# Kernel optimization log

Hardware: AMD Instinct MI355X
Metric: run time of the kernel (lower is better)

Reference implementation:

```python
import jax, jax.numpy as jnp
import numpy as np

N, E, F_IN, H, L = 1536, 49152, 27, 64, 32


def _ln(x, g, b, eps=1e-5):
    m = x.mean(-1, keepdims=True)
    v = ((x - m) ** 2).mean(-1, keepdims=True)
    return (x - m) * jax.lax.rsqrt(v + eps) * g + b


def _gatv2(x, src, dst, Wl, bl, Wr, br, att, bias, n):
    # PyG GATv2Conv, heads=1: alpha_ij = softmax_j( att . leaky_relu(Wl x_j + Wr x_i) )
    xl = x @ Wl + bl  # source transform [n,H]
    xr = x @ Wr + br  # target transform [n,H]
    e = jax.nn.leaky_relu(xl[src] + xr[dst], 0.2)  # [E',H]
    s = e @ att  # [E'] attention logits
    m = jax.ops.segment_max(s, dst, num_segments=n)
    w = jnp.exp(s - m[dst])
    denom = jax.ops.segment_sum(w, dst, num_segments=n)
    alpha = w / denom[dst]
    return jax.ops.segment_sum(alpha[:, None] * xl[src], dst, num_segments=n) + bias


def _model(x, eps_nodes, eps_graph, edge_index,
           Wl1, bl1, Wr1, br1, att1, bias1,
           Wl2, bl2, Wr2, br2, att2, bias2,
           Wnm, bnm, Wnv, bnv, Wgm, bgm, Wgv, bgv,
           Wd1, bd1, ln1_g, ln1_b, Wd2, bd2, ln2_g, ln2_b, Wd3, bd3,
           We1, be1, lne_g, lne_b, We2, be2,
           Wf1, bf1, lnf_g, lnf_b, Wf2, bf2):
    n = x.shape[0]
    loop = jnp.arange(n)
    src = jnp.concatenate([edge_index[0], loop])  # add self loops (PyG default)
    dst = jnp.concatenate([edge_index[1], loop])
    h = jax.nn.relu(_gatv2(x, src, dst, Wl1, bl1, Wr1, br1, att1, bias1, n))
    h = jax.nn.relu(_gatv2(h, src, dst, Wl2, bl2, Wr2, br2, att2, bias2, n))
    node_mu = h @ Wnm + bnm
    node_logvar = h @ Wnv + bnv
    gh = h.mean(0)
    graph_mu = gh @ Wgm + bgm
    graph_logvar = gh @ Wgv + bgv
    z = node_mu + eps_nodes * jnp.exp(0.5 * node_logvar)  # node reparam (training)
    _zg = graph_mu + eps_graph * jnp.exp(0.5 * graph_logvar)  # z_graph: computed, unused downstream as in source
    # dec_node_features MLP
    nf = _ln(jax.nn.relu(z @ Wd1 + bd1), ln1_g, ln1_b)
    nf = _ln(jax.nn.relu(nf @ Wd2 + bd2), ln2_g, ln2_b)
    nf = nf @ Wd3 + bd3  # [n, F_IN]
    # feature_refinement (node_embeddings = h is passed in forward)
    nf = _ln(jax.nn.relu(jnp.concatenate([nf, h], -1) @ Wf1 + bf1), lnf_g, lnf_b)
    node_features = nf @ Wf2 + bf2
    # edge_pred over all i<j pairs, vectorized (replaces the O(N^2) python loop)
    iu, ju = jnp.triu_indices(n, k=1)
    ei = jnp.concatenate([z[iu], z[ju]], -1)  # [P, 2L]
    eh = _ln(jax.nn.relu(ei @ We1 + be1), lne_g, lne_b)
    edge_logits = (eh @ We2 + be2)[:, 0]  # [P]
    return node_features, edge_logits, node_mu, node_logvar, graph_mu, graph_logvar


def setup_inputs() -> dict:
    key = jax.random.key(0)
    ki = iter(jax.random.split(key, 40))
    def W(fi, fo):
        return jax.random.normal(next(ki), (fi, fo), jnp.float32) / np.sqrt(fi)
    z64 = jnp.zeros((H,), jnp.float32)
    o64 = jnp.ones((H,), jnp.float32)
    zL = jnp.zeros((L,), jnp.float32)
    zF = jnp.zeros((F_IN,), jnp.float32)
    inp = {}
    inp["x"] = jax.random.normal(next(ki), (N, F_IN), jnp.float32)
    inp["edge_index"] = jax.random.randint(next(ki), (2, E), 0, N)
    inp["eps_nodes"] = jax.random.normal(next(ki), (N, L), jnp.float32)
    inp["eps_graph"] = jax.random.normal(next(ki), (L,), jnp.float32)
    inp.update(Wl1=W(F_IN, H), bl1=z64, Wr1=W(F_IN, H), br1=z64,
               att1=jax.random.normal(next(ki), (H,), jnp.float32) / np.sqrt(H), bias1=z64,
               Wl2=W(H, H), bl2=z64, Wr2=W(H, H), br2=z64,
               att2=jax.random.normal(next(ki), (H,), jnp.float32) / np.sqrt(H), bias2=z64)
    inp.update(Wnm=W(H, L), bnm=zL, Wnv=W(H, L), bnv=zL,
               Wgm=W(H, L), bgm=zL, Wgv=W(H, L), bgv=zL)
    inp.update(Wd1=W(L, H), bd1=z64, ln1_g=o64, ln1_b=z64,
               Wd2=W(H, H), bd2=z64, ln2_g=o64, ln2_b=z64,
               Wd3=W(H, F_IN), bd3=zF)
    inp.update(We1=W(2 * L, H), be1=z64, lne_g=o64, lne_b=z64,
               We2=W(H, 1), be2=jnp.zeros((1,), jnp.float32))
    inp.update(Wf1=W(F_IN + H, H), bf1=z64, lnf_g=o64, lnf_b=z64,
               Wf2=W(H, F_IN), bf2=zF)
    return inp


def reference(x, edge_index, eps_nodes, eps_graph,
              Wl1, bl1, Wr1, br1, att1, bias1,
              Wl2, bl2, Wr2, br2, att2, bias2,
              Wnm, bnm, Wnv, bnv, Wgm, bgm, Wgv, bgv,
              Wd1, bd1, ln1_g, ln1_b, Wd2, bd2, ln2_g, ln2_b, Wd3, bd3,
              We1, be1, lne_g, lne_b, We2, be2,
              Wf1, bf1, lnf_g, lnf_b, Wf2, bf2):
    return _model(x, eps_nodes, eps_graph, edge_index,
                  Wl1, bl1, Wr1, br1, att1, bias1,
                  Wl2, bl2, Wr2, br2, att2, bias2,
                  Wnm, bnm, Wnv, bnv, Wgm, bgm, Wgv, bgv,
                  Wd1, bd1, ln1_g, ln1_b, Wd2, bd2, ln2_g, ln2_b, Wd3, bd3,
                  We1, be1, lne_g, lne_b, We2, be2,
                  Wf1, bf1, lnf_g, lnf_b, Wf2, bf2)
```

## Files before the change

kernel.cpp:

```cpp
#include <hip/hip_runtime.h>

#define NN 1536
#define NE 49152
#define NM (NE + NN)
#define FIN 27
#define HD 64
#define LDIM 32
#define PP 1178880

#define EL_OFF  (NN*FIN)
#define MU_OFF  (EL_OFF + PP)
#define LV_OFF  (MU_OFF + NN*LDIM)
#define GMU_OFF (LV_OFF + NN*LDIM)
#define GLV_OFF (GMU_OFF + LDIM)

__device__ __forceinline__ float wsum(float v) {
#pragma unroll
  for (int m = 1; m < 64; m <<= 1) v += __shfl_xor(v, m, 64);
  return v;
}
__device__ __forceinline__ void wsum2(float& a, float& b) {
#pragma unroll
  for (int m = 1; m < 64; m <<= 1) {
    a += __shfl_xor(a, m, 64);
    b += __shfl_xor(b, m, 64);
  }
}
__device__ __forceinline__ float lnorm64(float x, float g, float b) {
  float s1 = x, s2 = x * x;
  wsum2(s1, s2);
  float mu = s1 * (1.0f / 64.0f);
  float var = fmaf(-mu, mu, s2 * (1.0f / 64.0f));
  return (x - mu) * rsqrtf(var + 1e-5f) * g + b;
}
__device__ __forceinline__ void cp4(float* dst, const float* __restrict__ src,
                                    int n4, int t) {
  const float4* s4 = (const float4*)src;
  float4* d4 = (float4*)dst;
  for (int e = t; e < n4; e += 256) d4[e] = s4[e];
}

template <int KIN, bool FUSE>
__global__ __launch_bounds__(256) void gvae_xform(
    const float* __restrict__ in, const float* __restrict__ Dn,
    const float* __restrict__ hbias,
    const float* __restrict__ Wl, const float* __restrict__ bl,
    const float* __restrict__ Wr, const float* __restrict__ br,
    float* __restrict__ xl, float* __restrict__ xr) {
  __shared__ __align__(16) float sWl[KIN * HD];
  __shared__ __align__(16) float sWr[KIN * HD];
  int t = threadIdx.x;
  cp4(sWl, Wl, KIN * 16, t);
  cp4(sWr, Wr, KIN * 16, t);
  int i = blockIdx.x * 4 + (t >> 6);
  int k = t & 63;
  float xv = (k < KIN) ? in[i * KIN + k] : 0.f;
  if (FUSE) xv = fmaxf(xv / Dn[i] + hbias[k], 0.f);
  float l0 = bl[k], l1 = 0.f, r0 = br[k], r1 = 0.f;
  __syncthreads();
#pragma unroll
  for (int a = 0; a < KIN; a += 2) {
    float xa = __shfl(xv, a, 64);
    l0 = fmaf(xa, sWl[a * HD + k], l0);
    r0 = fmaf(xa, sWr[a * HD + k], r0);
    if (a + 1 < KIN) {
      float xb = __shfl(xv, a + 1, 64);
      l1 = fmaf(xb, sWl[(a + 1) * HD + k], l1);
      r1 = fmaf(xb, sWr[(a + 1) * HD + k], r1);
    }
  }
  xl[i * HD + k] = l0 + l1;
  xr[i * HD + k] = r0 + r1;
}

__global__ __launch_bounds__(256) void gvae_edgepass(
    const int* __restrict__ ei,
    const float* __restrict__ xl, const float* __restrict__ xr,
    const float* __restrict__ att,
    float* __restrict__ A, float* __restrict__ D) {
  int m = blockIdx.x * 4 + (threadIdx.x >> 6);
  int lane = threadIdx.x & 63;
  int src, dst;
  if (m < NE) { src = ei[m]; dst = ei[NE + m]; }
  else        { src = m - NE; dst = m - NE; }
  float xls = xl[src * HD + lane];
  float e = xls + xr[dst * HD + lane];
  e = fmaxf(e, 0.2f * e);
  float w = expf(wsum(e * att[lane]));
  atomicAdd(&A[dst * HD + lane], w * xls);
  if (lane == 0) atomicAdd(&D[dst], w);
}

#define oNM 0
#define oNV 2048
#define oE1 4096
#define oD1 8192
#define oD2 10240
#define oD3 14336
#define oF1 16064
#define oF2 21888
#define SWTOT 23616

__global__ __launch_bounds__(256) void gvae_node(
    const float* __restrict__ A2, const float* __restrict__ D2,
    const float* __restrict__ bias2,
    const float* __restrict__ eps,
    const float* __restrict__ Wnm, const float* __restrict__ bnm,
    const float* __restrict__ Wnv, const float* __restrict__ bnv,
    const float* __restrict__ We1, const float* __restrict__ be1,
    const float* __restrict__ Wd1, const float* __restrict__ bd1,
    const float* __restrict__ g1, const float* __restrict__ b1,
    const float* __restrict__ Wd2, const float* __restrict__ bd2,
    const float* __restrict__ g2, const float* __restrict__ b2,
    const float* __restrict__ Wd3, const float* __restrict__ bd3,
    const float* __restrict__ Wf1, const float* __restrict__ bf1,
    const float* __restrict__ gf, const float* __restrict__ bfv,
    const float* __restrict__ Wf2, const float* __restrict__ bf2,
    float* __restrict__ uo, float* __restrict__ vo,
    float* __restrict__ gh, float* __restrict__ out) {
  __shared__ __align__(16) float sW[SWTOT];
  __shared__ float ghred[256];
  int t = threadIdx.x;
  cp4(sW + oNM, Wnm, 512, t);
  cp4(sW + oNV, Wnv, 512, t);
  cp4(sW + oE1, We1, 1024, t);
  cp4(sW + oD1, Wd1, 512, t);
  cp4(sW + oD2, Wd2, 1024, t);
  cp4(sW + oD3, Wd3, 432, t);
  cp4(sW + oF1, Wf1, 1456, t);
  cp4(sW + oF2, Wf2, 432, t);

  int i = blockIdx.x * 4 + (t >> 6);
  int k = t & 63;
  int kk = k & 31;
  int kc = (k < FIN) ? k : (FIN - 1);
  float h2k = fmaxf(A2[i * HD + k] / D2[i] + bias2[k], 0.f);
  ghred[t] = h2k;
  __syncthreads();
  if (t < 64) {
    float s = (ghred[t] + ghred[t + 64]) + (ghred[t + 128] + ghred[t + 192]);
    atomicAdd(&gh[t], s * (1.0f / NN));
  }

  const float* W = sW + ((k < 32) ? oNM : oNV);
  float c0 = (k < 32) ? bnm[kk] : bnv[kk];
  float c1 = 0.f, c2 = 0.f, c3 = 0.f;
#pragma unroll
  for (int a = 0; a < HD; a += 4) {
    c0 = fmaf(__shfl(h2k, a, 64),     W[a * LDIM + kk],       c0);
    c1 = fmaf(__shfl(h2k, a + 1, 64), W[(a + 1) * LDIM + kk], c1);
    c2 = fmaf(__shfl(h2k, a + 2, 64), W[(a + 2) * LDIM + kk], c2);
    c3 = fmaf(__shfl(h2k, a + 3, 64), W[(a + 3) * LDIM + kk], c3);
  }
  float acc = (c0 + c1) + (c2 + c3);
  if (k < 32) out[MU_OFF + i * LDIM + kk] = acc;
  else        out[LV_OFF + i * LDIM + kk] = acc;

  float lv = __shfl(acc, k + 32, 64);
  float zk = acc + eps[i * LDIM + kk] * expf(0.5f * lv);

  float u0 = be1[k], u1 = 0.f, v0 = 0.f, v1 = 0.f;
#pragma unroll
  for (int a = 0; a < LDIM; a += 2) {
    float za = __shfl(zk, a, 64);
    float zb = __shfl(zk, a + 1, 64);
    u0 = fmaf(za, sW[oE1 + a * HD + k], u0);
    u1 = fmaf(zb, sW[oE1 + (a + 1) * HD + k], u1);
    v0 = fmaf(za, sW[oE1 + (a + LDIM) * HD + k], v0);
    v1 = fmaf(zb, sW[oE1 + (a + 1 + LDIM) * HD + k], v1);
  }
  uo[i * HD + k] = u0 + u1;
  vo[i * HD + k] = v0 + v1;

  c0 = bd1[k]; c1 = 0.f; c2 = 0.f; c3 = 0.f;
#pragma unroll
  for (int a = 0; a < LDIM; a += 4) {
    c0 = fmaf(__shfl(zk, a, 64),     sW[oD1 + a * HD + k],       c0);
    c1 = fmaf(__shfl(zk, a + 1, 64), sW[oD1 + (a + 1) * HD + k], c1);
    c2 = fmaf(__shfl(zk, a + 2, 64), sW[oD1 + (a + 2) * HD + k], c2);
    c3 = fmaf(__shfl(zk, a + 3, 64), sW[oD1 + (a + 3) * HD + k], c3);
  }
  float nf1 = lnorm64(fmaxf((c0 + c1) + (c2 + c3), 0.f), g1[k], b1[k]);

  c0 = bd2[k]; c1 = 0.f; c2 = 0.f; c3 = 0.f;
#pragma unroll
  for (int a = 0; a < HD; a += 4) {
    c0 = fmaf(__shfl(nf1, a, 64),     sW[oD2 + a * HD + k],       c0);
    c1 = fmaf(__shfl(nf1, a + 1, 64), sW[oD2 + (a + 1) * HD + k], c1);
    c2 = fmaf(__shfl(nf1, a + 2, 64), sW[oD2 + (a + 2) * HD + k], c2);
    c3 = fmaf(__shfl(nf1, a + 3, 64), sW[oD2 + (a + 3) * HD + k], c3);
  }
  float nf2 = lnorm64(fmaxf((c0 + c1) + (c2 + c3), 0.f), g2[k], b2[k]);

  c0 = 0.f; c1 = 0.f; c2 = 0.f; c3 = 0.f;
#pragma unroll
  for (int a = 0; a < HD; a += 4) {
    c0 = fmaf(__shfl(nf2, a, 64),     sW[oD3 + a * FIN + kc],       c0);
    c1 = fmaf(__shfl(nf2, a + 1, 64), sW[oD3 + (a + 1) * FIN + kc], c1);
    c2 = fmaf(__shfl(nf2, a + 2, 64), sW[oD3 + (a + 2) * FIN + kc], c2);
    c3 = fmaf(__shfl(nf2, a + 3, 64), sW[oD3 + (a + 3) * FIN + kc], c3);
  }
  float nf3 = (k < FIN) ? ((c0 + c1) + (c2 + c3) + bd3[kc]) : 0.f;

  c0 = bf1[k]; c1 = 0.f; c2 = 0.f; c3 = 0.f;
#pragma unroll
  for (int j = 0; j < FIN; j++) {
    float nj = __shfl(nf3, j, 64);
    c0 = fmaf(nj, sW[oF1 + j * HD + k], c0);
  }
#pragma unroll
  for (int a = 0; a < HD; a += 4) {
    c0 = fmaf(__shfl(h2k, a, 64),     sW[oF1 + (FIN + a) * HD + k],     c0);
    c1 = fmaf(__shfl(h2k, a + 1, 64), sW[oF1 + (FIN + a + 1) * HD + k], c1);
    c2 = fmaf(__shfl(h2k, a + 2, 64), sW[oF1 + (FIN + a + 2) * HD + k], c2);
    c3 = fmaf(__shfl(h2k, a + 3, 64), sW[oF1 + (FIN + a + 3) * HD + k], c3);
  }
  float rr = lnorm64(fmaxf((c0 + c1) + (c2 + c3), 0.f), gf[k], bfv[k]);

  c0 = 0.f; c1 = 0.f; c2 = 0.f; c3 = 0.f;
#pragma unroll
  for (int a = 0; a < HD; a += 4) {
    c0 = fmaf(__shfl(rr, a, 64),     sW[oF2 + a * FIN + kc],       c0);
    c1 = fmaf(__shfl(rr, a + 1, 64), sW[oF2 + (a + 1) * FIN + kc], c1);
    c2 = fmaf(__shfl(rr, a + 2, 64), sW[oF2 + (a + 2) * FIN + kc], c2);
    c3 = fmaf(__shfl(rr, a + 3, 64), sW[oF2 + (a + 3) * FIN + kc], c3);
  }
  if (k < FIN) out[i * FIN + k] = (c0 + c1) + (c2 + c3) + bf2[kc];
}

__global__ void gvae_ghead(const float* __restrict__ gh,
                           const float* __restrict__ Wgm, const float* __restrict__ bgm,
                           const float* __restrict__ Wgv, const float* __restrict__ bgv,
                           float* __restrict__ out) {
  int k = threadIdx.x;
  int kk = k & 31;
  float ghk = gh[k];
  const float* W = (k < 32) ? Wgm : Wgv;
  float c0 = (k < 32) ? bgm[kk] : bgv[kk];
  float c1 = 0.f, c2 = 0.f, c3 = 0.f;
#pragma unroll
  for (int a = 0; a < HD; a += 4) {
    c0 = fmaf(__shfl(ghk, a, 64),     W[a * LDIM + kk],       c0);
    c1 = fmaf(__shfl(ghk, a + 1, 64), W[(a + 1) * LDIM + kk], c1);
    c2 = fmaf(__shfl(ghk, a + 2, 64), W[(a + 2) * LDIM + kk], c2);
    c3 = fmaf(__shfl(ghk, a + 3, 64), W[(a + 3) * LDIM + kk], c3);
  }
  float acc = (c0 + c1) + (c2 + c3);
  if (k < 32) out[GMU_OFF + kk] = acc;
  else        out[GLV_OFF + kk] = acc;
}

__global__ __launch_bounds__(256) void gvae_edge(
    const float* __restrict__ u, const float* __restrict__ v,
    const float* __restrict__ lng, const float* __restrict__ lnb,
    const float* __restrict__ w2, const float* __restrict__ be2,
    float* __restrict__ out) {
  int bj = blockIdx.x, bi = blockIdx.y;
  if (bi > bj) return;
  __shared__ float U[64 * 64];
  __shared__ float V[64 * 68];
  __shared__ float C[64];
  __shared__ float cc[2];
  int t = threadIdx.x;
  const float4* u4p = (const float4*)(u + bi * 64 * HD);
  const float4* v4p = (const float4*)(v + bj * 64 * HD);
#pragma unroll
  for (int it = 0; it < 4; ++it) {
    int r = t + it * 256;
    int row = r >> 4, q = r & 15;
    float4 uu = u4p[r];
    *(float4*)&U[row * 64 + q * 4] = uu;
    float4 vv = v4p[r];
    *(float4*)&V[row * 68 + q * 4] = vv;
  }
  if (t < 64) {
    float ck = lng[t] * w2[t];
    C[t] = ck;
    float cb = lnb[t] * w2[t];
    float sC = wsum(ck);
    float sB = wsum(cb);
    if (t == 0) { cc[0] = sC; cc[1] = sB + be2[0]; }
  }
  __syncthreads();
  float C1 = cc[0], C0 = cc[1];

  int w = t >> 6, lane = t & 63;
  float S1[16], S2[16], Sc[16];
#pragma unroll
  for (int ii = 0; ii < 16; ii++) { S1[ii] = 0.f; S2[ii] = 0.f; Sc[ii] = 0.f; }
  const float* Ub = &U[(w * 16) * 64];
  for (int k4 = 0; k4 < 16; k4++) {
    float4 v4 = *(const float4*)&V[lane * 68 + k4 * 4];
    float4 c4 = *(const float4*)&C[k4 * 4];
#pragma unroll
    for (int ii = 0; ii < 16; ii++) {
      float4 u4 = *(const float4*)&Ub[ii * 64 + k4 * 4];
      float t0 = fmaxf(u4.x + v4.x, 0.f);
      float t1 = fmaxf(u4.y + v4.y, 0.f);
      float t2 = fmaxf(u4.z + v4.z, 0.f);
      float t3 = fmaxf(u4.w + v4.w, 0.f);
      S1[ii] += (t0 + t1) + (t2 + t3);
      S2[ii] = fmaf(t0, t0, fmaf(t1, t1, fmaf(t2, t2, fmaf(t3, t3, S2[ii]))));
      Sc[ii] = fmaf(t0, c4.x, fmaf(t1, c4.y, fmaf(t2, c4.z, fmaf(t3, c4.w, Sc[ii]))));
    }
  }
  int j = bj * 64 + lane;
  const float inv64 = 1.0f / 64.0f;
#pragma unroll
  for (int ii = 0; ii < 16; ii++) {
    int i = bi * 64 + w * 16 + ii;
    if (j > i) {
      int pbase = i * (2 * NN - i - 1) / 2 - i - 1;
      float mu = S1[ii] * inv64;
      float var = fmaf(-mu, mu, S2[ii] * inv64);
      float logit = (Sc[ii] - mu * C1) * rsqrtf(var + 1e-5f) + C0;
      out[pbase + j] = logit;
    }
  }
}

extern "C" void kernel_launch(void* const* d_in, const int* in_sizes, int n_in,
                              void* d_out, int out_size, void* d_ws, size_t ws_size,
                              hipStream_t stream) {
  const float* x    = (const float*)d_in[0];
  const int*   ei   = (const int*)d_in[1];
  const float* eps  = (const float*)d_in[2];
  const float* Wl1  = (const float*)d_in[4];
  const float* bl1  = (const float*)d_in[5];
  const float* Wr1  = (const float*)d_in[6];
  const float* br1  = (const float*)d_in[7];
  const float* att1 = (const float*)d_in[8];
  const float* bias1= (const float*)d_in[9];
  const float* Wl2  = (const float*)d_in[10];
  const float* bl2  = (const float*)d_in[11];
  const float* Wr2  = (const float*)d_in[12];
  const float* br2  = (const float*)d_in[13];
  const float* att2 = (const float*)d_in[14];
  const float* bias2= (const float*)d_in[15];
  const float* Wnm  = (const float*)d_in[16];
  const float* bnm  = (const float*)d_in[17];
  const float* Wnv  = (const float*)d_in[18];
  const float* bnv  = (const float*)d_in[19];
  const float* Wgm  = (const float*)d_in[20];
  const float* bgm  = (const float*)d_in[21];
  const float* Wgv  = (const float*)d_in[22];
  const float* bgv  = (const float*)d_in[23];
  const float* Wd1  = (const float*)d_in[24];
  const float* bd1  = (const float*)d_in[25];
  const float* ln1g = (const float*)d_in[26];
  const float* ln1b = (const float*)d_in[27];
  const float* Wd2  = (const float*)d_in[28];
  const float* bd2  = (const float*)d_in[29];
  const float* ln2g = (const float*)d_in[30];
  const float* ln2b = (const float*)d_in[31];
  const float* Wd3  = (const float*)d_in[32];
  const float* bd3  = (const float*)d_in[33];
  const float* We1  = (const float*)d_in[34];
  const float* be1  = (const float*)d_in[35];
  const float* lneg = (const float*)d_in[36];
  const float* lneb = (const float*)d_in[37];
  const float* We2  = (const float*)d_in[38];
  const float* be2  = (const float*)d_in[39];
  const float* Wf1  = (const float*)d_in[40];
  const float* bf1  = (const float*)d_in[41];
  const float* lnfg = (const float*)d_in[42];
  const float* lnfb = (const float*)d_in[43];
  const float* Wf2  = (const float*)d_in[44];
  const float* bf2  = (const float*)d_in[45];
  float* out = (float*)d_out;

  float* fb  = (float*)d_ws;
  float* xl1 = fb;
  float* xr1 = xl1 + NN * HD;
  float* xl2 = xr1 + NN * HD;
  float* xr2 = xl2 + NN * HD;
  float* uu  = xr2 + NN * HD;
  float* vv  = uu  + NN * HD;
  float* A1  = vv  + NN * HD;
  float* A2  = A1  + NN * HD;
  float* D1  = A2  + NN * HD;
  float* D2  = D1  + NN;
  float* gh  = D2  + NN;
  size_t zbytes = (size_t)(2 * NN * HD + 2 * NN + HD) * sizeof(float);

  hipMemsetAsync(A1, 0, zbytes, stream);

  gvae_xform<FIN, false><<<NN / 4, 256, 0, stream>>>(x, nullptr, nullptr,
                                                     Wl1, bl1, Wr1, br1, xl1, xr1);
  gvae_edgepass<<<NM / 4, 256, 0, stream>>>(ei, xl1, xr1, att1, A1, D1);
  gvae_xform<HD, true><<<NN / 4, 256, 0, stream>>>(A1, D1, bias1,
                                                   Wl2, bl2, Wr2, br2, xl2, xr2);
  gvae_edgepass<<<NM / 4, 256, 0, stream>>>(ei, xl2, xr2, att2, A2, D2);

  gvae_node<<<NN / 4, 256, 0, stream>>>(A2, D2, bias2, eps,
      Wnm, bnm, Wnv, bnv, We1, be1,
      Wd1, bd1, ln1g, ln1b, Wd2, bd2, ln2g, ln2b, Wd3, bd3,
      Wf1, bf1, lnfg, lnfb, Wf2, bf2,
      uu, vv, gh, out);
  gvae_ghead<<<1, 64, 0, stream>>>(gh, Wgm, bgm, Wgv, bgv, out);
  gvae_edge<<<dim3(24, 24), 256, 0, stream>>>(uu, vv, lneg, lneb, We2, be2, out + EL_OFF);
}
```

Measured before the change: 259.7 us.

## Fuse all stages into one persistent cooperative kernel with grid syncs

Measured after the change: 990.6 us. 3.81x slower.

```diff
diff --git a/kernel.cpp b/kernel.cpp
--- a/kernel.cpp
+++ b/kernel.cpp
@@ -1,4 +1,7 @@
 #include <hip/hip_runtime.h>
+#include <hip/hip_cooperative_groups.h>
+
+namespace cg = cooperative_groups;
 
 #define NN 1536
 #define NE 49152
@@ -33,370 +36,345 @@
   float var = fmaf(-mu, mu, s2 * (1.0f / 64.0f));
   return (x - mu) * rsqrtf(var + 1e-5f) * g + b;
 }
-__device__ __forceinline__ void cp4(float* dst, const float* __restrict__ src,
-                                    int n4, int t) {
-  const float4* s4 = (const float4*)src;
-  float4* d4 = (float4*)dst;
-  for (int e = t; e < n4; e += 256) d4[e] = s4[e];
-}
-
-template <int KIN, bool FUSE>
-__global__ __launch_bounds__(256) void gvae_xform(
-    const float* __restrict__ in, const float* __restrict__ Dn,
-    const float* __restrict__ hbias,
-    const float* __restrict__ Wl, const float* __restrict__ bl,
-    const float* __restrict__ Wr, const float* __restrict__ br,
-    float* __restrict__ xl, float* __restrict__ xr) {
-  __shared__ __align__(16) float sWl[KIN * HD];
-  __shared__ __align__(16) float sWr[KIN * HD];
-  int t = threadIdx.x;
-  cp4(sWl, Wl, KIN * 16, t);
-  cp4(sWr, Wr, KIN * 16, t);
-  int i = blockIdx.x * 4 + (t >> 6);
-  int k = t & 63;
-  float xv = (k < KIN) ? in[i * KIN + k] : 0.f;
-  if (FUSE) xv = fmaxf(xv / Dn[i] + hbias[k], 0.f);
-  float l0 = bl[k], l1 = 0.f, r0 = br[k], r1 = 0.f;
-  __syncthreads();
-#pragma unroll
-  for (int a = 0; a < KIN; a += 2) {
-    float xa = __shfl(xv, a, 64);
-    l0 = fmaf(xa, sWl[a * HD + k], l0);
-    r0 = fmaf(xa, sWr[a * HD + k], r0);
-    if (a + 1 < KIN) {
-      float xb = __shfl(xv, a + 1, 64);
-      l1 = fmaf(xb, sWl[(a + 1) * HD + k], l1);
-      r1 = fmaf(xb, sWr[(a + 1) * HD + k], r1);
-    }
-  }
-  xl[i * HD + k] = l0 + l1;
-  xr[i * HD + k] = r0 + r1;
-}
-
-__global__ __launch_bounds__(256) void gvae_edgepass(
-    const int* __restrict__ ei,
-    const float* __restrict__ xl, const float* __restrict__ xr,
-    const float* __restrict__ att,
-    float* __restrict__ A, float* __restrict__ D) {
-  int m = blockIdx.x * 4 + (threadIdx.x >> 6);
-  int lane = threadIdx.x & 63;
-  int src, dst;
-  if (m < NE) { src = ei[m]; dst = ei[NE + m]; }
-  else        { src = m - NE; dst = m - NE; }
-  float xls = xl[src * HD + lane];
-  float e = xls + xr[dst * HD + lane];
-  e = fmaxf(e, 0.2f * e);
-  float w = expf(wsum(e * att[lane]));
-  atomicAdd(&A[dst * HD + lane], w * xls);
-  if (lane == 0) atomicAdd(&D[dst], w);
-}
-
-#define oNM 0
-#define oNV 2048
-#define oE1 4096
-#define oD1 8192
-#define oD2 10240
-#define oD3 14336
-#define oF1 16064
-#define oF2 21888
-#define SWTOT 23616
-
-__global__ __launch_bounds__(256) void gvae_node(
-    const float* __restrict__ A2, const float* __restrict__ D2,
-    const float* __restrict__ bias2,
-    const float* __restrict__ eps,
-    const float* __restrict__ Wnm, const float* __restrict__ bnm,
-    const float* __restrict__ Wnv, const float* __restrict__ bnv,
-    const float* __restrict__ We1, const float* __restrict__ be1,
-    const float* __restrict__ Wd1, const float* __restrict__ bd1,
-    const float* __restrict__ g1, const float* __restrict__ b1,
-    const float* __restrict__ Wd2, const float* __restrict__ bd2,
-    const float* __restrict__ g2, const float* __restrict__ b2,
-    const float* __restrict__ Wd3, const float* __restrict__ bd3,
-    const float* __restrict__ Wf1, const float* __restrict__ bf1,
-    const float* __restrict__ gf, const float* __restrict__ bfv,
-    const float* __restrict__ Wf2, const float* __restrict__ bf2,
-    float* __restrict__ uo, float* __restrict__ vo,
-    float* __restrict__ gh, float* __restrict__ out) {
-  __shared__ __align__(16) float sW[SWTOT];
-  __shared__ float ghred[256];
-  int t = threadIdx.x;
-  cp4(sW + oNM, Wnm, 512, t);
-  cp4(sW + oNV, Wnv, 512, t);
-  cp4(sW + oE1, We1, 1024, t);
-  cp4(sW + oD1, Wd1, 512, t);
-  cp4(sW + oD2, Wd2, 1024, t);
-  cp4(sW + oD3, Wd3, 432, t);
-  cp4(sW + oF1, Wf1, 1456, t);
-  cp4(sW + oF2, Wf2, 432, t);
-
-  int i = blockIdx.x * 4 + (t >> 6);
-  int k = t & 63;
-  int kk = k & 31;
-  int kc = (k < FIN) ? k : (FIN - 1);
-  float h2k = fmaxf(A2[i * HD + k] / D2[i] + bias2[k], 0.f);
-  ghred[t] = h2k;
-  __syncthreads();
+
+struct GP {
+  const float* x; const int* ei; const float* eps;
+  const float *Wl1, *bl1, *Wr1, *br1, *att1, *bias1;
+  const float *Wl2, *bl2, *Wr2, *br2, *att2, *bias2;
+  const float *Wnm, *bnm, *Wnv, *bnv, *Wgm, *bgm, *Wgv, *bgv;
+  const float *Wd1, *bd1, *g1, *b1, *Wd2, *bd2, *g2, *b2, *Wd3, *bd3;
+  const float *We1, *be1, *lng, *lnb, *w2, *be2;
+  const float *Wf1, *bf1, *gf, *bfv, *Wf2, *bf2;
+  float *xl1, *xr1, *xl2, *xr2, *uu, *vv;
+  float *A1, *A2, *D1, *D2, *gh;
+  float* out;
+};
+
+__global__ __launch_bounds__(256, 4) void gvae_mono(GP p) {
+  cg::grid_group grid = cg::this_grid();
+  __shared__ __align__(16) float sh[8516];
+  const int t = threadIdx.x, b = blockIdx.x;
+  const int NB = gridDim.x;
+  const int wv = t >> 6, lane = t & 63;
+  const int WSTRIDE = NB * 4;
+
+  {
+    float4* z4 = (float4*)p.A1;
+    const int nz4 = (2 * NN * HD + 2 * NN + HD) / 4;
+    float4 zz = {0.f, 0.f, 0.f, 0.f};
+    for (int e = b * 256 + t; e < nz4; e += NB * 256) z4[e] = zz;
+    float bl = p.bl1[lane], br = p.br1[lane];
+    for (int i = b + NB * wv; i < NN; i += WSTRIDE) {
+      float xv = (lane < FIN) ? p.x[i * FIN + lane] : 0.f;
+      float l0 = bl, l1 = 0.f, r0 = br, r1 = 0.f;
+#pragma unroll
+      for (int a = 0; a < FIN; a += 2) {
+        float xa = __shfl(xv, a, 64);
+        l0 = fmaf(xa, p.Wl1[a * HD + lane], l0);
+        r0 = fmaf(xa, p.Wr1[a * HD + lane], r0);
+        if (a + 1 < FIN) {
+          float xb = __shfl(xv, a + 1, 64);
+          l1 = fmaf(xb, p.Wl1[(a + 1) * HD + lane], l1);
+          r1 = fmaf(xb, p.Wr1[(a + 1) * HD + lane], r1);
+        }
+      }
+      p.xl1[i * HD + lane] = l0 + l1;
+      p.xr1[i * HD + lane] = r0 + r1;
+    }
+  }
+  __threadfence();
+  grid.sync();
+
+  {
+    float ak = p.att1[lane];
+    for (int m = b + NB * wv; m < NM; m += WSTRIDE) {
+      int src, dst;
+      if (m < NE) { src = p.ei[m]; dst = p.ei[NE + m]; }
+      else        { src = m - NE; dst = src; }
+      float xls = p.xl1[src * HD + lane];
+      float e = xls + p.xr1[dst * HD + lane];
+      e = fmaxf(e, 0.2f * e);
+      float w = expf(wsum(e * ak));
+      atomicAdd(&p.A1[dst * HD + lane], w * xls);
+      if (lane == 0) atomicAdd(&p.D1[dst], w);
+    }
+  }
+  __threadfence();
+  grid.sync();
+
+  {
+    float hb = p.bias1[lane], bl = p.bl2[lane], br = p.br2[lane];
+    for (int i = b + NB * wv; i < NN; i += WSTRIDE) {
+      float xv = fmaxf(p.A1[i * HD + lane] / p.D1[i] + hb, 0.f);
+      float l0 = bl, l1 = 0.f, r0 = br, r1 = 0.f;
+#pragma unroll
+      for (int a = 0; a < HD; a += 2) {
+        float xa = __shfl(xv, a, 64);
+        float xb = __shfl(xv, a + 1, 64);
+        l0 = fmaf(xa, p.Wl2[a * HD + lane], l0);
+        r0 = fmaf(xa, p.Wr2[a * HD + lane], r0);
+        l1 = fmaf(xb, p.Wl2[(a + 1) * HD + lane], l1);
+        r1 = fmaf(xb, p.Wr2[(a + 1) * HD + lane], r1);
+      }
+      p.xl2[i * HD + lane] = l0 + l1;
+      p.xr2[i * HD + lane] = r0 + r1;
+    }
+  }
+  __threadfence();
+  grid.sync();
+
+  {
+    float ak = p.att2[lane];
+    for (int m = b + NB * wv; m < NM; m += WSTRIDE) {
+      int src, dst;
+      if (m < NE) { src = p.ei[m]; dst = p.ei[NE + m]; }
+      else        { src = m - NE; dst = src; }
+      float xls = p.xl2[src * HD + lane];
+      float e = xls + p.xr2[dst * HD + lane];
+      e = fmaxf(e, 0.2f * e);
+      float w = expf(wsum(e * ak));
+      atomicAdd(&p.A2[dst * HD + lane], w * xls);
+      if (lane == 0) atomicAdd(&p.D2[dst], w);
+    }
+  }
+  __threadfence();
+  grid.sync();
+
+  {
+    const int k = lane, kk = k & 31;
+    const int kc = (k < FIN) ? k : (FIN - 1);
+    for (int i = b + NB * wv; i < NN; i += WSTRIDE) {
+      float h2k = fmaxf(p.A2[i * HD + k] / p.D2[i] + p.bias2[k], 0.f);
+      atomicAdd(&p.gh[k], h2k * (1.0f / NN));
+
+      const float* W = (k < 32) ? p.Wnm : p.Wnv;
+      float c0 = (k < 32) ? p.bnm[kk] : p.bnv[kk];
+      float c1 = 0.f, c2 = 0.f, c3 = 0.f;
+#pragma unroll
+      for (int a = 0; a < HD; a += 4) {
+        c0 = fmaf(__shfl(h2k, a, 64),     W[a * LDIM + kk],       c0);
+        c1 = fmaf(__shfl(h2k, a + 1, 64), W[(a + 1) * LDIM + kk], c1);
+        c2 = fmaf(__shfl(h2k, a + 2, 64), W[(a + 2) * LDIM + kk], c2);
+        c3 = fmaf(__shfl(h2k, a + 3, 64), W[(a + 3) * LDIM + kk], c3);
+      }
+      float acc = (c0 + c1) + (c2 + c3);
+      if (k < 32) p.out[MU_OFF + i * LDIM + kk] = acc;
+      else        p.out[LV_OFF + i * LDIM + kk] = acc;
+
+      float lv = __shfl(acc, k + 32, 64);
+      float zk = acc + p.eps[i * LDIM + kk] * expf(0.5f * lv);
+
+      float u0 = p.be1[k], u1 = 0.f, v0 = 0.f, v1 = 0.f;
+#pragma unroll
+      for (int a = 0; a < LDIM; a += 2) {
+        float za = __shfl(zk, a, 64);
+        float zb = __shfl(zk, a + 1, 64);
+        u0 = fmaf(za, p.We1[a * HD + k], u0);
+        u1 = fmaf(zb, p.We1[(a + 1) * HD + k], u1);
+        v0 = fmaf(za, p.We1[(a + LDIM) * HD + k], v0);
+        v1 = fmaf(zb, p.We1[(a + 1 + LDIM) * HD + k], v1);
+      }
+      p.uu[i * HD + k] = u0 + u1;
+      p.vv[i * HD + k] = v0 + v1;
+
+      c0 = p.bd1[k]; c1 = 0.f; c2 = 0.f; c3 = 0.f;
+#pragma unroll
+      for (int a = 0; a < LDIM; a += 4) {
+        c0 = fmaf(__shfl(zk, a, 64),     p.Wd1[a * HD + k],       c0);
+        c1 = fmaf(__shfl(zk, a + 1, 64), p.Wd1[(a + 1) * HD + k], c1);
+        c2 = fmaf(__shfl(zk, a + 2, 64), p.Wd1[(a + 2) * HD + k], c2);
+        c3 = fmaf(__shfl(zk, a + 3, 64), p.Wd1[(a + 3) * HD + k], c3);
+      }
+      float nf1 = lnorm64(fmaxf((c0 + c1) + (c2 + c3), 0.f), p.g1[k], p.b1[k]);
+
+      c0 = p.bd2[k]; c1 = 0.f; c2 = 0.f; c3 = 0.f;
+#pragma unroll
+      for (int a = 0; a < HD; a += 4) {
+        c0 = fmaf(__shfl(nf1, a, 64),     p.Wd2[a * HD + k],       c0);
+        c1 = fmaf(__shfl(nf1, a + 1, 64), p.Wd2[(a + 1) * HD + k], c1);
+        c2 = fmaf(__shfl(nf1, a + 2, 64), p.Wd2[(a + 2) * HD + k], c2);
+        c3 = fmaf(__shfl(nf1, a + 3, 64), p.Wd2[(a + 3) * HD + k], c3);
+      }
+      float nf2 = lnorm64(fmaxf((c0 + c1) + (c2 + c3), 0.f), p.g2[k], p.b2[k]);
+
+      c0 = 0.f; c1 = 0.f; c2 = 0.f; c3 = 0.f;
+#pragma unroll
+      for (int a = 0; a < HD; a += 4) {
+        c0 = fmaf(__shfl(nf2, a, 64),     p.Wd3[a * FIN + kc],       c0);
+        c1 = fmaf(__shfl(nf2, a + 1, 64), p.Wd3[(a + 1) * FIN + kc], c1);
+        c2 = fmaf(__shfl(nf2, a + 2, 64), p.Wd3[(a + 2) * FIN + kc], c2);
+        c3 = fmaf(__shfl(nf2, a + 3, 64), p.Wd3[(a + 3) * FIN + kc], c3);
+      }
+      float nf3 = (k < FIN) ? ((c0 + c1) + (c2 + c3) + p.bd3[kc]) : 0.f;
+
+      c0 = p.bf1[k]; c1 = 0.f; c2 = 0.f; c3 = 0.f;
+#pragma unroll
+      for (int j = 0; j < FIN; j++) {
+        float nj = __shfl(nf3, j, 64);
+        c0 = fmaf(nj, p.Wf1[j * HD + k], c0);
+      }
+#pragma unroll
+      for (int a = 0; a < HD; a += 4) {
+        c0 = fmaf(__shfl(h2k, a, 64),     p.Wf1[(FIN + a) * HD + k],     c0);
+        c1 = fmaf(__shfl(h2k, a + 1, 64), p.Wf1[(FIN + a + 1) * HD + k], c1);
+        c2 = fmaf(__shfl(h2k, a + 2, 64), p.Wf1[(FIN + a + 2) * HD + k], c2);
+        c3 = fmaf(__shfl(h2k, a + 3, 64), p.Wf1[(FIN + a + 3) * HD + k], c3);
+      }
+      float rr = lnorm64(fmaxf((c0 + c1) + (c2 + c3), 0.f), p.gf[k], p.bfv[k]);
+
+      c0 = 0.f; c1 = 0.f; c2 = 0.f; c3 = 0.f;
+#pragma unroll
+      for (int a = 0; a < HD; a += 4) {
+        c0 = fmaf(__shfl(rr, a, 64),     p.Wf2[a * FIN + kc],       c0);
+        c1 = fmaf(__shfl(rr, a + 1, 64), p.Wf2[(a + 1) * FIN + kc], c1);
+        c2 = fmaf(__shfl(rr, a + 2, 64), p.Wf2[(a + 2) * FIN + kc], c2);
+        c3 = fmaf(__shfl(rr, a + 3, 64), p.Wf2[(a + 3) * FIN + kc], c3);
+      }
+      if (k < FIN) p.out[i * FIN + k] = (c0 + c1) + (c2 + c3) + p.bf2[kc];
+    }
+  }
+  __threadfence();
+  grid.sync();
+
+  if (b == 0 && wv == 3) {
+    int kk = lane & 31;
+    float ghk = p.gh[lane];
+    const float* W = (lane < 32) ? p.Wgm : p.Wgv;
+    float c0 = (lane < 32) ? p.bgm[kk] : p.bgv[kk];
+    float c1 = 0.f, c2 = 0.f, c3 = 0.f;
+#pragma unroll
+    for (int a = 0; a < HD; a += 4) {
+      c0 = fmaf(__shfl(ghk, a, 64),     W[a * LDIM + kk],       c0);
+      c1 = fmaf(__shfl(ghk, a + 1, 64), W[(a + 1) * LDIM + kk], c1);
+      c2 = fmaf(__shfl(ghk, a + 2, 64), W[(a + 2) * LDIM + kk], c2);
+      c3 = fmaf(__shfl(ghk, a + 3, 64), W[(a + 3) * LDIM + kk], c3);
+    }
+    float acc = (c0 + c1) + (c2 + c3);
+    if (lane < 32) p.out[GMU_OFF + kk] = acc;
+    else           p.out[GLV_OFF + kk] = acc;
+  }
+
+  float* U  = sh;
+  float* V  = sh + 4096;
+  float* C  = sh + 4096 + 64 * 68;
+  float* cc = C + 64;
   if (t < 64) {
-    float s = (ghred[t] + ghred[t + 64]) + (ghred[t + 128] + ghred[t + 192]);
-    atomicAdd(&gh[t], s * (1.0f / NN));
-  }
-
-  const float* W = sW + ((k < 32) ? oNM : oNV);
-  float c0 = (k < 32) ? bnm[kk] : bnv[kk];
-  float c1 = 0.f, c2 = 0.f, c3 = 0.f;
-#pragma unroll
-  for (int a = 0; a < HD; a += 4) {
-    c0 = fmaf(__shfl(h2k, a, 64),     W[a * LDIM + kk],       c0);
-    c1 = fmaf(__shfl(h2k, a + 1, 64), W[(a + 1) * LDIM + kk], c1);
-    c2 = fmaf(__shfl(h2k, a + 2, 64), W[(a + 2) * LDIM + kk], c2);
-    c3 = fmaf(__shfl(h2k, a + 3, 64), W[(a + 3) * LDIM + kk], c3);
-  }
-  float acc = (c0 + c1) + (c2 + c3);
-  if (k < 32) out[MU_OFF + i * LDIM + kk] = acc;
-  else        out[LV_OFF + i * LDIM + kk] = acc;
-
-  float lv = __shfl(acc, k + 32, 64);
-  float zk = acc + eps[i * LDIM + kk] * expf(0.5f * lv);
-
-  float u0 = be1[k], u1 = 0.f, v0 = 0.f, v1 = 0.f;
-#pragma unroll
-  for (int a = 0; a < LDIM; a += 2) {
-    float za = __shfl(zk, a, 64);
-    float zb = __shfl(zk, a + 1, 64);
-    u0 = fmaf(za, sW[oE1 + a * HD + k], u0);
-    u1 = fmaf(zb, sW[oE1 + (a + 1) * HD + k], u1);
-    v0 = fmaf(za, sW[oE1 + (a + LDIM) * HD + k], v0);
-    v1 = fmaf(zb, sW[oE1 + (a + 1 + LDIM) * HD + k], v1);
-  }
-  uo[i * HD + k] = u0 + u1;
-  vo[i * HD + k] = v0 + v1;
-
-  c0 = bd1[k]; c1 = 0.f; c2 = 0.f; c3 = 0.f;
-#pragma unroll
-  for (int a = 0; a < LDIM; a += 4) {
-    c0 = fmaf(__shfl(zk, a, 64),     sW[oD1 + a * HD + k],       c0);
-    c1 = fmaf(__shfl(zk, a + 1, 64), sW[oD1 + (a + 1) * HD + k], c1);
-    c2 = fmaf(__shfl(zk, a + 2, 64), sW[oD1 + (a + 2) * HD + k], c2);
-    c3 = fmaf(__shfl(zk, a + 3, 64), sW[oD1 + (a + 3) * HD + k], c3);
-  }
-  float nf1 = lnorm64(fmaxf((c0 + c1) + (c2 + c3), 0.f), g1[k], b1[k]);
-
-  c0 = bd2[k]; c1 = 0.f; c2 = 0.f; c3 = 0.f;
-#pragma unroll
-  for (int a = 0; a < HD; a += 4) {
-    c0 = fmaf(__shfl(nf1, a, 64),     sW[oD2 + a * HD + k],       c0);
-    c1 = fmaf(__shfl(nf1, a + 1, 64), sW[oD2 + (a + 1) * HD + k], c1);
-    c2 = fmaf(__shfl(nf1, a + 2, 64), sW[oD2 + (a + 2) * HD + k], c2);
-    c3 = fmaf(__shfl(nf1, a + 3, 64), sW[oD2 + (a + 3) * HD + k], c3);
-  }
-  float nf2 = lnorm64(fmaxf((c0 + c1) + (c2 + c3), 0.f), g2[k], b2[k]);
-
-  c0 = 0.f; c1 = 0.f; c2 = 0.f; c3 = 0.f;
-#pragma unroll
-  for (int a = 0; a < HD; a += 4) {
-    c0 = fmaf(__shfl(nf2, a, 64),     sW[oD3 + a * FIN + kc],       c0);
-    c1 = fmaf(__shfl(nf2, a + 1, 64), sW[oD3 + (a + 1) * FIN + kc], c1);
-    c2 = fmaf(__shfl(nf2, a + 2, 64), sW[oD3 + (a + 2) * FIN + kc], c2);
-    c3 = fmaf(__shfl(nf2, a + 3, 64), sW[oD3 + (a + 3) * FIN + kc], c3);
-  }
-  float nf3 = (k < FIN) ? ((c0 + c1) + (c2 + c3) + bd3[kc]) : 0.f;
-
-  c0 = bf1[k]; c1 = 0.f; c2 = 0.f; c3 = 0.f;
-#pragma unroll
-  for (int j = 0; j < FIN; j++) {
-    float nj = __shfl(nf3, j, 64);
-    c0 = fmaf(nj, sW[oF1 + j * HD + k], c0);
-  }
-#pragma unroll
-  for (int a = 0; a < HD; a += 4) {
-    c0 = fmaf(__shfl(h2k, a, 64),     sW[oF1 + (FIN + a) * HD + k],     c0);
-    c1 = fmaf(__shfl(h2k, a + 1, 64), sW[oF1 + (FIN + a + 1) * HD + k], c1);
-    c2 = fmaf(__shfl(h2k, a + 2, 64), sW[oF1 + (FIN + a + 2) * HD + k], c2);
-    c3 = fmaf(__shfl(h2k, a + 3, 64), sW[oF1 + (FIN + a + 3) * HD + k], c3);
-  }
-  float rr = lnorm64(fmaxf((c0 + c1) + (c2 + c3), 0.f), gf[k], bfv[k]);
-
-  c0 = 0.f; c1 = 0.f; c2 = 0.f; c3 = 0.f;
-#pragma unroll
-  for (int a = 0; a < HD; a += 4) {
-    c0 = fmaf(__shfl(rr, a, 64),     sW[oF2 + a * FIN + kc],       c0);
-    c1 = fmaf(__shfl(rr, a + 1, 64), sW[oF2 + (a + 1) * FIN + kc], c1);
-    c2 = fmaf(__shfl(rr, a + 2, 64), sW[oF2 + (a + 2) * FIN + kc], c2);
-    c3 = fmaf(__shfl(rr, a + 3, 64), sW[oF2 + (a + 3) * FIN + kc], c3);
-  }
-  if (k < FIN) out[i * FIN + k] = (c0 + c1) + (c2 + c3) + bf2[kc];
-}
-
-__global__ void gvae_ghead(const float* __restrict__ gh,
-                           const float* __restrict__ Wgm, const float* __restrict__ bgm,
-                           const float* __restrict__ Wgv, const float* __restrict__ bgv,
-                           float* __restrict__ out) {
-  int k = threadIdx.x;
-  int kk = k & 31;
-  float ghk = gh[k];
-  const float* W = (k < 32) ? Wgm : Wgv;
-  float c0 = (k < 32) ? bgm[kk] : bgv[kk];
-  float c1 = 0.f, c2 = 0.f, c3 = 0.f;
-#pragma unroll
-  for (int a = 0; a < HD; a += 4) {
-    c0 = fmaf(__shfl(ghk, a, 64),     W[a * LDIM + kk],       c0);
-    c1 = fmaf(__shfl(ghk, a + 1, 64), W[(a + 1) * LDIM + kk], c1);
-    c2 = fmaf(__shfl(ghk, a + 2, 64), W[(a + 2) * LDIM + kk], c2);
-    c3 = fmaf(__shfl(ghk, a + 3, 64), W[(a + 3) * LDIM + kk], c3);
-  }
-  float acc = (c0 + c1) + (c2 + c3);
-  if (k < 32) out[GMU_OFF + kk] = acc;
-  else        out[GLV_OFF + kk] = acc;
-}
-
-__global__ __launch_bounds__(256) void gvae_edge(
-    const float* __restrict__ u, const float* __restrict__ v,
-    const float* __restrict__ lng, const float* __restrict__ lnb,
-    const float* __restrict__ w2, const float* __restrict__ be2,
-    float* __restrict__ out) {
-  int bj = blockIdx.x, bi = blockIdx.y;
-  if (bi > bj) return;
-  __shared__ float U[64 * 64];
-  __shared__ float V[64 * 68];
-  __shared__ float C[64];
-  __shared__ float cc[2];
-  int t = threadIdx.x;
-  const float4* u4p = (const float4*)(u + bi * 64 * HD);
-  const float4* v4p = (const float4*)(v + bj * 64 * HD);
-#pragma unroll
-  for (int it = 0; it < 4; ++it) {
-    int r = t + it * 256;
-    int row = r >> 4, q = r & 15;
-    float4 uu = u4p[r];
-    *(float4*)&U[row * 64 + q * 4] = uu;
-    float4 vv = v4p[r];
-    *(float4*)&V[row * 68 + q * 4] = vv;
-  }
-  if (t < 64) {
-    float ck = lng[t] * w2[t];
+    float ck = p.lng[t] * p.w2[t];
     C[t] = ck;
-    float cb = lnb[t] * w2[t];
+    float cb = p.lnb[t] * p.w2[t];
     float sC = wsum(ck);
     float sB = wsum(cb);
-    if (t == 0) { cc[0] = sC; cc[1] = sB + be2[0]; }
-  }
-  __syncthreads();
-  float C1 = cc[0], C0 = cc[1];
-
-  int w = t >> 6, lane = t & 63;
-  float S1[16], S2[16], Sc[16];
-#pragma unroll
-  for (int ii = 0; ii < 16; ii++) { S1[ii] = 0.f; S2[ii] = 0.f; Sc[ii] = 0.f; }
-  const float* Ub = &U[(w * 16) * 64];
-  for (int k4 = 0; k4 < 16; k4++) {
-    float4 v4 = *(const float4*)&V[lane * 68 + k4 * 4];
-    float4 c4 = *(const float4*)&C[k4 * 4];
+    if (t == 0) { cc[0] = sC; cc[1] = sB + p.be2[0]; }
+  }
+
+  for (int tt = b; tt < 300; tt += NB) {
+    int rem = tt, bi = 0;
+    while (rem >= 24 - bi) { rem -= 24 - bi; bi++; }
+    int bj = bi + rem;
+    const float4* u4p = (const float4*)(p.uu + bi * 64 * HD);
+    const float4* v4p = (const float4*)(p.vv + bj * 64 * HD);
+#pragma unroll
+    for (int it = 0; it < 4; ++it) {
+      int r = t + it * 256;
+      int row = r >> 4, q = r & 15;
+      float4 uu4 = u4p[r];
+      *(float4*)&U[row * 64 + q * 4] = uu4;
+      float4 vv4 = v4p[r];
+      *(float4*)&V[row * 68 + q * 4] = vv4;
+    }
+    __syncthreads();
+    float C1 = cc[0], C0 = cc[1];
+
+    float S1[16], S2[16], Sc[16];
+#pragma unroll
+    for (int ii = 0; ii < 16; ii++) { S1[ii] = 0.f; S2[ii] = 0.f; Sc[ii] = 0.f; }
+    const float* Ub = &U[(wv * 16) * 64];
+    for (int k4 = 0; k4 < 16; k4++) {
+      float4 v4 = *(const float4*)&V[lane * 68 + k4 * 4];
+      float4 c4 = *(const float4*)&C[k4 * 4];
+#pragma unroll
+      for (int ii = 0; ii < 16; ii++) {
+        float4 u4 = *(const float4*)&Ub[ii * 64 + k4 * 4];
+        float t0 = fmaxf(u4.x + v4.x, 0.f);
+        float t1 = fmaxf(u4.y + v4.y, 0.f);
+        float t2 = fmaxf(u4.z + v4.z, 0.f);
+        float t3 = fmaxf(u4.w + v4.w, 0.f);
+        S1[ii] += (t0 + t1) + (t2 + t3);
+        S2[ii] = fmaf(t0, t0, fmaf(t1, t1, fmaf(t2, t2, fmaf(t3, t3, S2[ii]))));
+        Sc[ii] = fmaf(t0, c4.x, fmaf(t1, c4.y, fmaf(t2, c4.z, fmaf(t3, c4.w, Sc[ii]))));
+      }
+    }
+    int j = bj * 64 + lane;
+    const float inv64 = 1.0f / 64.0f;
 #pragma unroll
     for (int ii = 0; ii < 16; ii++) {
-      float4 u4 = *(const float4*)&Ub[ii * 64 + k4 * 4];
-      float t0 = fmaxf(u4.x + v4.x, 0.f);
-      float t1 = fmaxf(u4.y + v4.y, 0.f);
-      float t2 = fmaxf(u4.z + v4.z, 0.f);
-      float t3 = fmaxf(u4.w + v4.w, 0.f);
-      S1[ii] += (t0 + t1) + (t2 + t3);
-      S2[ii] = fmaf(t0, t0, fmaf(t1, t1, fmaf(t2, t2, fmaf(t3, t3, S2[ii]))));
-      Sc[ii] = fmaf(t0, c4.x, fmaf(t1, c4.y, fmaf(t2, c4.z, fmaf(t3, c4.w, Sc[ii]))));
-    }
-  }
-  int j = bj * 64 + lane;
-  const float inv64 = 1.0f / 64.0f;
-#pragma unroll
-  for (int ii = 0; ii < 16; ii++) {
-    int i = bi * 64 + w * 16 + ii;
-    if (j > i) {
-      int pbase = i * (2 * NN - i - 1) / 2 - i - 1;
-      float mu = S1[ii] * inv64;
-      float var = fmaf(-mu, mu, S2[ii] * inv64);
-      float logit = (Sc[ii] - mu * C1) * rsqrtf(var + 1e-5f) + C0;
-      out[pbase + j] = logit;
-    }
+      int i = bi * 64 + wv * 16 + ii;
+      if (j > i) {
+        int pbase = i * (2 * NN - i - 1) / 2 - i - 1;
+        float mu = S1[ii] * inv64;
+        float var = fmaf(-mu, mu, S2[ii] * inv64);
+        float logit = (Sc[ii] - mu * C1) * rsqrtf(var + 1e-5f) + C0;
+        p.out[EL_OFF + pbase + j] = logit;
+      }
+    }
+    __syncthreads();
   }
 }
 
 extern "C" void kernel_launch(void* const* d_in, const int* in_sizes, int n_in,
                               void* d_out, int out_size, void* d_ws, size_t ws_size,
                               hipStream_t stream) {
-  const float* x    = (const float*)d_in[0];
-  const int*   ei   = (const int*)d_in[1];
-  const float* eps  = (const float*)d_in[2];
-  const float* Wl1  = (const float*)d_in[4];
-  const float* bl1  = (const float*)d_in[5];
-  const float* Wr1  = (const float*)d_in[6];
-  const float* br1  = (const float*)d_in[7];
-  const float* att1 = (const float*)d_in[8];
-  const float* bias1= (const float*)d_in[9];
-  const float* Wl2  = (const float*)d_in[10];
-  const float* bl2  = (const float*)d_in[11];
-  const float* Wr2  = (const float*)d_in[12];
-  const float* br2  = (const float*)d_in[13];
-  const float* att2 = (const float*)d_in[14];
-  const float* bias2= (const float*)d_in[15];
-  const float* Wnm  = (const float*)d_in[16];
-  const float* bnm  = (const float*)d_in[17];
-  const float* Wnv  = (const float*)d_in[18];
-  const float* bnv  = (const float*)d_in[19];
-  const float* Wgm  = (const float*)d_in[20];
-  const float* bgm  = (const float*)d_in[21];
-  const float* Wgv  = (const float*)d_in[22];
-  const float* bgv  = (const float*)d_in[23];
-  const float* Wd1  = (const float*)d_in[24];
-  const float* bd1  = (const float*)d_in[25];
-  const float* ln1g = (const float*)d_in[26];
-  const float* ln1b = (const float*)d_in[27];
-  const float* Wd2  = (const float*)d_in[28];
-  const float* bd2  = (const float*)d_in[29];
-  const float* ln2g = (const float*)d_in[30];
-  const float* ln2b = (const float*)d_in[31];
-  const float* Wd3  = (const float*)d_in[32];
-  const float* bd3  = (const float*)d_in[33];
-  const float* We1  = (const float*)d_in[34];
-  const float* be1  = (const float*)d_in[35];
-  const float* lneg = (const float*)d_in[36];
-  const float* lneb = (const float*)d_in[37];
-  const float* We2  = (const float*)d_in[38];
-  const float* be2  = (const float*)d_in[39];
-  const float* Wf1  = (const float*)d_in[40];
-  const float* bf1  = (const float*)d_in[41];
-  const float* lnfg = (const float*)d_in[42];
-  const float* lnfb = (const float*)d_in[43];
-  const float* Wf2  = (const float*)d_in[44];
-  const float* bf2  = (const float*)d_in[45];
-  float* out = (float*)d_out;
-
-  float* fb  = (float*)d_ws;
-  float* xl1 = fb;
-  float* xr1 = xl1 + NN * HD;
-  float* xl2 = xr1 + NN * HD;
-  float* xr2 = xl2 + NN * HD;
-  float* uu  = xr2 + NN * HD;
-  float* vv  = uu  + NN * HD;
-  float* A1  = vv  + NN * HD;
-  float* A2  = A1  + NN * HD;
-  float* D1  = A2  + NN * HD;
-  float* D2  = D1  + NN;
-  float* gh  = D2  + NN;
-  size_t zbytes = (size_t)(2 * NN * HD + 2 * NN + HD) * sizeof(float);
-
-  hipMemsetAsync(A1, 0, zbytes, stream);
-
-  gvae_xform<FIN, false><<<NN / 4, 256, 0, stream>>>(x, nullptr, nullptr,
-                                                     Wl1, bl1, Wr1, br1, xl1, xr1);
-  gvae_edgepass<<<NM / 4, 256, 0, stream>>>(ei, xl1, xr1, att1, A1, D1);
-  gvae_xform<HD, true><<<NN / 4, 256, 0, stream>>>(A1, D1, bias1,
-                                                   Wl2, bl2, Wr2, br2, xl2, xr2);
-  gvae_edgepass<<<NM / 4, 256, 0, stream>>>(ei, xl2, xr2, att2, A2, D2);
-
-  gvae_node<<<NN / 4, 256, 0, stream>>>(A2, D2, bias2, eps,
-      Wnm, bnm, Wnv, bnv, We1, be1,
-      Wd1, bd1, ln1g, ln1b, Wd2, bd2, ln2g, ln2b, Wd3, bd3,
-      Wf1, bf1, lnfg, lnfb, Wf2, bf2,
-      uu, vv, gh, out);
-  gvae_ghead<<<1, 64, 0, stream>>>(gh, Wgm, bgm, Wgv, bgv, out);
-  gvae_edge<<<dim3(24, 24), 256, 0, stream>>>(uu, vv, lneg, lneb, We2, be2, out + EL_OFF);
-}
+  GP p;
+  p.x    = (const float*)d_in[0];
+  p.ei   = (const int*)d_in[1];
+  p.eps  = (const float*)d_in[2];
+  p.Wl1  = (const float*)d_in[4];  p.bl1 = (const float*)d_in[5];
+  p.Wr1  = (const float*)d_in[6];  p.br1 = (const float*)d_in[7];
+  p.att1 = (const float*)d_in[8];  p.bias1 = (const float*)d_in[9];
+  p.Wl2  = (const float*)d_in[10]; p.bl2 = (const float*)d_in[11];
+  p.Wr2  = (const float*)d_in[12]; p.br2 = (const float*)d_in[13];
+  p.att2 = (const float*)d_in[14]; p.bias2 = (const float*)d_in[15];
+  p.Wnm  = (const float*)d_in[16]; p.bnm = (const float*)d_in[17];
+  p.Wnv  = (const float*)d_in[18]; p.bnv = (const float*)d_in[19];
+  p.Wgm  = (const float*)d_in[20]; p.bgm = (const float*)d_in[21];
+  p.Wgv  = (const float*)d_in[22]; p.bgv = (const float*)d_in[23];
+  p.Wd1  = (const float*)d_in[24]; p.bd1 = (const float*)d_in[25];
+  p.g1   = (const float*)d_in[26]; p.b1  = (const float*)d_in[27];
+  p.Wd2  = (const float*)d_in[28]; p.bd2 = (const float*)d_in[29];
+  p.g2   = (const float*)d_in[30]; p.b2  = (const float*)d_in[31];
+  p.Wd3  = (const float*)d_in[32]; p.bd3 = (const float*)d_in[33];
+  p.We1  = (const float*)d_in[34]; p.be1 = (const float*)d_in[35];
+  p.lng  = (const float*)d_in[36]; p.lnb = (const float*)d_in[37];
+  p.w2   = (const float*)d_in[38]; p.be2 = (const float*)d_in[39];
+  p.Wf1  = (const float*)d_in[40]; p.bf1 = (const float*)d_in[41];
+  p.gf   = (const float*)d_in[42]; p.bfv = (const float*)d_in[43];
+  p.Wf2  = (const float*)d_in[44]; p.bf2 = (const float*)d_in[45];
+  p.out  = (float*)d_out;
+
+  float* fb = (float*)d_ws;
+  p.xl1 = fb;
+  p.xr1 = p.xl1 + NN * HD;
+  p.xl2 = p.xr1 + NN * HD;
+  p.xr2 = p.xl2 + NN * HD;
+  p.uu  = p.xr2 + NN * HD;
+  p.vv  = p.uu  + NN * HD;
+  p.A1  = p.vv  + NN * HD;
+  p.A2  = p.A1  + NN * HD;
+  p.D1  = p.A2  + NN * HD;
+  p.D2  = p.D1  + NN;
+  p.gh  = p.D2  + NN;
+
+  int dev = 0;
+  hipGetDevice(&dev);
+  int numCU = 256;
+  hipDeviceGetAttribute(&numCU, hipDeviceAttributeMultiprocessorCount, dev);
+  int maxb = 0;
+  hipOccupancyMaxActiveBlocksPerMultiprocessor(&maxb, (const void*)gvae_mono, 256, 0);
+  if (maxb < 1) maxb = 1;
+  int nb = maxb * numCU;
+  if (nb > 2048) nb = 2048;
+
+  void* kargs[] = { (void*)&p };
+  hipLaunchCooperativeKernel((const void*)gvae_mono, dim3(nb), dim3(256),
+                             kargs, 0, stream);
+}
```
